# Optimization experiments

Measured on AMD Instinct MI355X. Metric: run time of the kernel, lower is better.

## Reference

```python
import jax, jax.numpy as jnp
import numpy as np

D = 1024
LD = 64
NTR = 8192
NT = 8192
DY = 128

def setup_inputs() -> dict:
    key = jax.random.key(0)
    k1, k2, k3, k4 = jax.random.split(key, 4)
    xtr = jax.random.normal(k1, (NTR, D), dtype=jnp.float32)
    ytr = jax.random.normal(k2, (NTR, DY), dtype=jnp.float32)
    xt = jax.random.normal(k3, (NT, D), dtype=jnp.float32)
    A = jax.random.normal(k4, (D, LD), dtype=jnp.float32) / (D ** 0.5)
    return {"xtr": xtr, "ytr": ytr, "xt": xt, "A": A}

def reference(xtr, ytr, xt, A):
    # mean-center both train and test features with the train mean
    mu = jnp.mean(xtr, axis=0, keepdims=True)          # [1, d]
    qtr = (xtr - mu) @ A                                # [Ntr, ld]
    qt = (xt - mu) @ A                                  # [Nt, ld]
    scores = jnp.einsum('nl,ml->nm', qt, qtr)           # [Nt, Ntr]
    E = jax.nn.softmax(scores, axis=1)                  # row-wise softmax over train points
    return E @ ytr                                      # [Nt, dy]
```

## Files before the change

kernel.cpp:

```cpp
#include <hip/hip_runtime.h>
#include <hip/hip_bf16.h>

#define D    1024
#define LD   64
#define NTR  8192
#define NT   8192
#define DY   128

#define SHIFT 40.0f
#define NCHUNK 8
#define CHUNK (NTR / NCHUNK)

typedef __attribute__((ext_vector_type(8))) short bf16x8;
typedef __attribute__((ext_vector_type(4))) short short4_;
typedef __attribute__((ext_vector_type(4))) float f4;

static __device__ __forceinline__ short f2bf(float f) {
    __hip_bfloat16 h = __float2bfloat16(f);
    short s; __builtin_memcpy(&s, &h, 2); return s;
}
static __device__ __forceinline__ float bf2f(short s) {
    __hip_bfloat16 h; __builtin_memcpy(&h, &s, 2); return __bfloat162float(h);
}

static __device__ __forceinline__ void gload_lds16(const void* g, void* l) {
    __builtin_amdgcn_global_load_lds(
        (const __attribute__((address_space(1))) unsigned int*)g,
        (__attribute__((address_space(3))) unsigned int*)l,
        16, 0, 0);
}

__global__ __launch_bounds__(256) void prep_all(const float* __restrict__ A,
                                                const float* __restrict__ ytr,
                                                short* __restrict__ AThi,
                                                short* __restrict__ ATlo,
                                                short* __restrict__ vtile) {
    __shared__ float tile[64][65];
    int b = blockIdx.x;
    if (b < 64) {
        int k = b * 16 + (threadIdx.x >> 4);
        int c0 = (threadIdx.x & 15) * 4;
        f4 a = *(const f4*)&A[(long)k * LD + c0];
        #pragma unroll
        for (int j = 0; j < 4; ++j) {
            int c = c0 + j;
            short hi = f2bf(a[j]);
            AThi[(long)c * D + k] = hi;
            ATlo[(long)c * D + k] = f2bf(a[j] - bf2f(hi));
        }
    } else {
        int bz = b - 64;
        int t0 = (bz & 127) * 64;
        int d0 = (bz >> 7) * 64;
        int c = threadIdx.x & 63;
        int r4 = threadIdx.x >> 6;
        #pragma unroll
        for (int i = 0; i < 16; ++i) {
            int r = i * 4 + r4;
            tile[r][c] = ytr[(long)(t0 + r) * DY + d0 + c];
        }
        __syncthreads();
        #pragma unroll
        for (int i = 0; i < 16; ++i) {
            int r = i * 4 + r4;
            int t = t0 + c;
            int dy = d0 + r;
            long idx = (long)(t >> 5) * 4096 + (long)dy * 32
                     + ((((t >> 3) & 3) ^ (dy & 3)) << 3) + (t & 7);
            vtile[idx] = f2bf(tile[c][r]);
        }
    }
}

__global__ __launch_bounds__(256) void proj_mfma(const float* __restrict__ xt,
                                                 const float* __restrict__ xtr,
                                                 const short* __restrict__ AThi,
                                                 const short* __restrict__ ATlo,
                                                 short* __restrict__ qt_hi,
                                                 short* __restrict__ qt_lo,
                                                 short* __restrict__ ktr_hi,
                                                 short* __restrict__ ktr_lo) {
    __shared__ __align__(16) float xbuf[2][1024];

    int tid = threadIdx.x;
    int wave = tid >> 6;
    int lane = tid & 63;
    int quad = lane >> 4;
    int l16 = lane & 15;

    int b = blockIdx.x;
    bool is_test = b < (NT / 16);
    int row0 = (is_test ? b : b - NT / 16) * 16;
    const float* x = is_test ? xt : xtr;

    int lr = wave * 4 + (lane >> 4);
    int cg = (lane & 15) ^ (lr & 7);
    const float* xsrc = x + (long)(row0 + lr) * D + cg * 4;
    float* ldst = &xbuf[0][wave * 256];

    const short* bhrow = AThi + (long)(wave * 16 + l16) * D + quad * 8;
    const short* blrow = ATlo + (long)(wave * 16 + l16) * D + quad * 8;

    f4 acc = (f4){0.f, 0.f, 0.f, 0.f};

    int pr0 = ((quad * 2) ^ (l16 & 7)) * 4;
    int pr1 = (((quad * 2) | 1) ^ (l16 & 7)) * 4;

    gload_lds16(xsrc, ldst);
    __syncthreads();

    #pragma unroll 1
    for (int s = 0; s < 16; ++s) {
        int cur = s & 1;
        if (s < 15)
            gload_lds16(xsrc + (s + 1) * 64, &xbuf[cur ^ 1][wave * 256]);

        const float* xrow = &xbuf[cur][l16 * 64];
        bf16x8 ah[2], al[2];
        #pragma unroll
        for (int h = 0; h < 2; ++h) {
            f4 v0 = *(const f4*)(xrow + h * 32 + pr0);
            f4 v1 = *(const f4*)(xrow + h * 32 + pr1);
            #pragma unroll
            for (int e = 0; e < 4; ++e) {
                short hi0 = f2bf(v0[e]);
                short hi1 = f2bf(v1[e]);
                ah[h][e]     = hi0;
                ah[h][e + 4] = hi1;
                al[h][e]     = f2bf(v0[e] - bf2f(hi0));
                al[h][e + 4] = f2bf(v1[e] - bf2f(hi1));
            }
        }
        int k0 = s * 64;
        bf16x8 bh0 = *(const bf16x8*)(bhrow + k0);
        bf16x8 bh1 = *(const bf16x8*)(bhrow + k0 + 32);
        bf16x8 bl0 = *(const bf16x8*)(blrow + k0);
        bf16x8 bl1 = *(const bf16x8*)(blrow + k0 + 32);
        acc = __builtin_amdgcn_mfma_f32_16x16x32_bf16(ah[0], bh0, acc, 0, 0, 0);
        acc = __builtin_amdgcn_mfma_f32_16x16x32_bf16(al[0], bh0, acc, 0, 0, 0);
        acc = __builtin_amdgcn_mfma_f32_16x16x32_bf16(ah[0], bl0, acc, 0, 0, 0);
        acc = __builtin_amdgcn_mfma_f32_16x16x32_bf16(ah[1], bh1, acc, 0, 0, 0);
        acc = __builtin_amdgcn_mfma_f32_16x16x32_bf16(al[1], bh1, acc, 0, 0, 0);
        acc = __builtin_amdgcn_mfma_f32_16x16x32_bf16(ah[1], bl1, acc, 0, 0, 0);

        __syncthreads();
    }


    int col = wave * 16 + l16;
    #pragma unroll
    for (int r = 0; r < 4; ++r) {
        int grow = row0 + quad * 4 + r;
        float qv = acc[r];
        short hi = f2bf(qv);
        short lo = f2bf(qv - bf2f(hi));
        if (is_test) {
            qt_hi[(long)grow * LD + col] = hi;
            qt_lo[(long)grow * LD + col] = lo;
        } else {
            int tl = grow & 31;
            long idx = (long)(grow >> 5) * 2048 + tl * 64
                     + ((((col >> 3) ^ (tl & 7))) << 3) + (col & 7);
            ktr_hi[idx] = hi;
            ktr_lo[idx] = lo;
        }
    }
}

__global__ __launch_bounds__(256) void muA_kernel(const short* __restrict__ ktr_hi,
                                                  const short* __restrict__ ktr_lo,
                                                  float* __restrict__ muA) {
    __shared__ float red[4][64];
    int l = threadIdx.x & 63;
    int g = threadIdx.x >> 6;
    float s = 0.f;
    #pragma unroll 2
    for (int tt = 0; tt < 4; ++tt) {
        long tb = (long)(blockIdx.x * 4 + tt) * 2048;
        #pragma unroll
        for (int tl = g * 8; tl < g * 8 + 8; ++tl) {
            long idx = tb + tl * 64 + ((((l >> 3) ^ (tl & 7))) << 3) + (l & 7);
            s += bf2f(ktr_hi[idx]) + bf2f(ktr_lo[idx]);
        }
    }
    red[g][l] = s;
    __syncthreads();
    if (threadIdx.x < 64)
        atomicAdd(&muA[l], (red[0][l] + red[1][l] + red[2][l] + red[3][l]) *
                               (1.0f / (float)NTR));
}

__global__ __launch_bounds__(256) void c_kernel(const short* __restrict__ ktr_hi,
                                                const short* __restrict__ ktr_lo,
                                                const float* __restrict__ muA,
                                                float* __restrict__ cc) {
    int t = blockIdx.x * 256 + threadIdx.x;
    int tl = t & 31;
    long rb = (long)(t >> 5) * 2048 + tl * 64;
    float s = SHIFT;
    #pragma unroll
    for (int c = 0; c < 8; ++c) {
        int pos = (c ^ (tl & 7)) << 3;
        bf16x8 h8 = *(const bf16x8*)&ktr_hi[rb + pos];
        bf16x8 l8 = *(const bf16x8*)&ktr_lo[rb + pos];
        f4 m0 = *(const f4*)&muA[c * 8];
        f4 m1 = *(const f4*)&muA[c * 8 + 4];
        #pragma unroll
        for (int j = 0; j < 4; ++j) {
            s += (bf2f(h8[j]) + bf2f(l8[j])) * m0[j];
            s += (bf2f(h8[j + 4]) + bf2f(l8[j + 4])) * m1[j];
        }
    }
    cc[t] = s;
}

__global__ __launch_bounds__(256, 2) void flash_kernel(const short* __restrict__ qt_hi,
                                                       const short* __restrict__ qt_lo,
                                                       const short* __restrict__ ksw_hi,
                                                       const short* __restrict__ ksw_lo,
                                                       const short* __restrict__ vtile,
                                                       const float* __restrict__ cc,
                                                       float* __restrict__ Opart,
                                                       float* __restrict__ Lpart) {
    __shared__ __align__(16) short kbh[2][2048];
    __shared__ __align__(16) short kbl[2][2048];
    __shared__ __align__(16) short vbuf[2][4096];
    __shared__ __align__(16) short ptile[4][1280];

    int tid = threadIdx.x;
    int wave = tid >> 6;
    int lane = tid & 63;
    int quad = lane >> 4;
    int l16 = lane & 15;

    int kc = blockIdx.x & 7;
    int qi = blockIdx.x >> 3;
    int q0w = qi * 128 + wave * 32;
    int tile0 = kc * 32;
    int kc0 = kc * CHUNK;

    int soff = wave * 512 + lane * 8;
    int ldso = wave * 512;

    bf16x8 qh[2][2], ql[2][2];
    #pragma unroll
    for (int rt = 0; rt < 2; ++rt) {
        const short* qrh = qt_hi + (long)(q0w + rt * 16 + l16) * LD + quad * 8;
        const short* qrl = qt_lo + (long)(q0w + rt * 16 + l16) * LD + quad * 8;
        qh[rt][0] = *(const bf16x8*)qrh;
        qh[rt][1] = *(const bf16x8*)(qrh + 32);
        ql[rt][0] = *(const bf16x8*)qrl;
        ql[rt][1] = *(const bf16x8*)(qrl + 32);
    }

    bf16x8 onef;
    #pragma unroll
    for (int i = 0; i < 8; ++i) onef[i] = (short)0x3F80;

    f4 Ov[2][8];
    f4 Lv[2];
    #pragma unroll
    for (int rt = 0; rt < 2; ++rt) {
        Lv[rt] = (f4){0.f, 0.f, 0.f, 0.f};
        #pragma unroll
        for (int jt = 0; jt < 8; ++jt) Ov[rt][jt] = (f4){0.f, 0.f, 0.f, 0.f};
    }

    short* myp = &ptile[wave][0];
    const int p0 = ((quad ^ (l16 & 7)) << 3);
    const int pv = ((quad ^ (l16 & 3)) << 3);

    gload_lds16(ksw_hi + (long)tile0 * 2048 + soff, &kbh[0][ldso]);
    gload_lds16(ksw_lo + (long)tile0 * 2048 + soff, &kbl[0][ldso]);
    gload_lds16(vtile + (long)tile0 * 4096 + soff, &vbuf[0][ldso]);
    gload_lds16(vtile + (long)tile0 * 4096 + 2048 + soff, &vbuf[0][2048 + ldso]);
    __syncthreads();

    #pragma unroll 1
    for (int it = 0; it < 32; ++it) {
        int cur = it & 1;

        f4 cv[2];
        #pragma unroll
        for (int tt = 0; tt < 2; ++tt)
            cv[tt] = *(const f4*)&cc[kc0 + it * 32 + tt * 16 + quad * 4];

        if (it < 31) {
            int nb = cur ^ 1;
            long tb = (long)(tile0 + it + 1);
            gload_lds16(ksw_hi + tb * 2048 + soff, &kbh[nb][ldso]);
            gload_lds16(ksw_lo + tb * 2048 + soff, &kbl[nb][ldso]);
            gload_lds16(vtile + tb * 4096 + soff, &vbuf[nb][ldso]);
            gload_lds16(vtile + tb * 4096 + 2048 + soff, &vbuf[nb][2048 + ldso]);
        }

        bf16x8 kh[2][2], kl[2][2];
        #pragma unroll
        for (int tt = 0; tt < 2; ++tt) {
            int rb = (tt * 16 + l16) * 64;
            kh[tt][0] = *(const bf16x8*)&kbh[cur][rb + p0];
            kh[tt][1] = *(const bf16x8*)&kbh[cur][rb + (p0 ^ 32)];
            kl[tt][0] = *(const bf16x8*)&kbl[cur][rb + p0];
            kl[tt][1] = *(const bf16x8*)&kbl[cur][rb + (p0 ^ 32)];
        }

        f4 s[2][2];
        #pragma unroll
        for (int rt = 0; rt < 2; ++rt) {
            #pragma unroll
            for (int tt = 0; tt < 2; ++tt) {
                f4 a = (f4){0.f, 0.f, 0.f, 0.f};
                a = __builtin_amdgcn_mfma_f32_16x16x32_bf16(kh[tt][0], qh[rt][0], a, 0, 0, 0);
                a = __builtin_amdgcn_mfma_f32_16x16x32_bf16(kh[tt][0], ql[rt][0], a, 0, 0, 0);
                a = __builtin_amdgcn_mfma_f32_16x16x32_bf16(kh[tt][1], qh[rt][1], a, 0, 0, 0);
                a = __builtin_amdgcn_mfma_f32_16x16x32_bf16(kh[tt][1], ql[rt][1], a, 0, 0, 0);
                a = __builtin_amdgcn_mfma_f32_16x16x32_bf16(kl[tt][0], qh[rt][0], a, 0, 0, 0);
                a = __builtin_amdgcn_mfma_f32_16x16x32_bf16(kl[tt][1], qh[rt][1], a, 0, 0, 0);
                s[rt][tt] = a;
            }
        }

        #pragma unroll
        for (int rt = 0; rt < 2; ++rt) {
            #pragma unroll
            for (int tt = 0; tt < 2; ++tt) {
                short4_ p4;
                p4[0] = f2bf(__expf(s[rt][tt][0] - cv[tt][0]));
                p4[1] = f2bf(__expf(s[rt][tt][1] - cv[tt][1]));
                p4[2] = f2bf(__expf(s[rt][tt][2] - cv[tt][2]));
                p4[3] = f2bf(__expf(s[rt][tt][3] - cv[tt][3]));
                *(short4_*)&myp[(rt * 16 + l16) * 40 + tt * 16 + quad * 4] = p4;
            }
        }

        bf16x8 vf[8];
        #pragma unroll
        for (int jt = 0; jt < 8; ++jt)
            vf[jt] = *(const bf16x8*)&vbuf[cur][(jt * 16 + l16) * 32 + pv];
        #pragma unroll
        for (int rt = 0; rt < 2; ++rt) {
            bf16x8 pf = *(const bf16x8*)&myp[(rt * 16 + l16) * 40 + quad * 8];
            #pragma unroll
            for (int jt = 0; jt < 8; ++jt)
                Ov[rt][jt] = __builtin_amdgcn_mfma_f32_16x16x32_bf16(pf, vf[jt], Ov[rt][jt], 0, 0, 0);
            Lv[rt] = __builtin_amdgcn_mfma_f32_16x16x32_bf16(pf, onef, Lv[rt], 0, 0, 0);
        }

        __syncthreads();
    }

    long ob = (long)kc * NT;
    #pragma unroll
    for (int rt = 0; rt < 2; ++rt) {
        #pragma unroll
        for (int jt = 0; jt < 8; ++jt) {
            #pragma unroll
            for (int r = 0; r < 4; ++r)
                Opart[(ob + q0w + rt * 16 + quad * 4 + r) * DY + jt * 16 + l16] =
                    Ov[rt][jt][r];
        }
        if (l16 == 0) {
            #pragma unroll
            for (int r = 0; r < 4; ++r)
                Lpart[ob + q0w + rt * 16 + quad * 4 + r] = Lv[rt][r];
        }
    }
}

__global__ __launch_bounds__(256) void finalize_kernel(const float* __restrict__ Opart,
                                                       const float* __restrict__ Lpart,
                                                       float* __restrict__ out) {
    long i = ((long)blockIdx.x * 256 + threadIdx.x) * 8;
    long row = i >> 7;
    float L = 0.f;
    f4 a = (f4){0.f, 0.f, 0.f, 0.f};
    f4 b = (f4){0.f, 0.f, 0.f, 0.f};
    #pragma unroll
    for (int kc = 0; kc < NCHUNK; ++kc) {
        L += Lpart[(long)kc * NT + row];
        const float* p = &Opart[((long)kc * NT) * DY + i];
        a += *(const f4*)p;
        b += *(const f4*)(p + 4);
    }
    float linv = 1.0f / L;
    a *= linv; b *= linv;
    *(f4*)&out[i] = a;
    *(f4*)&out[i + 4] = b;
}

extern "C" void kernel_launch(void* const* d_in, const int* in_sizes, int n_in,
                              void* d_out, int out_size, void* d_ws, size_t ws_size,
                              hipStream_t stream) {
    const float* xtr = (const float*)d_in[0];
    const float* ytr = (const float*)d_in[1];
    const float* xt  = (const float*)d_in[2];
    const float* A   = (const float*)d_in[3];
    float* out = (float*)d_out;

    char* w = (char*)d_ws;
    float* muA   = (float*)w; w += 4096;
    float* cc    = (float*)w; w += (size_t)NTR * 4;
    float* Lpart = (float*)w; w += (size_t)NCHUNK * NT * 4;
    float* Opart = (float*)w; w += (size_t)NCHUNK * NT * DY * 4;
    short* AThi  = (short*)w; w += (size_t)LD * D * 2;
    short* ATlo  = (short*)w; w += (size_t)LD * D * 2;
    short* qt_hi  = (short*)w; w += (size_t)NT * LD * 2;
    short* qt_lo  = (short*)w; w += (size_t)NT * LD * 2;
    short* ksw_hi = (short*)w; w += (size_t)NTR * LD * 2;
    short* ksw_lo = (short*)w; w += (size_t)NTR * LD * 2;
    short* vtile  = (short*)w; w += (size_t)DY * NTR * 2;
    (void)ws_size; (void)in_sizes; (void)n_in; (void)out_size;

    hipMemsetAsync(muA, 0, 4096, stream);
    prep_all<<<320, 256, 0, stream>>>(A, ytr, AThi, ATlo, vtile);
    proj_mfma<<<1024, 256, 0, stream>>>(xt, xtr, AThi, ATlo,
                                        qt_hi, qt_lo, ksw_hi, ksw_lo);
    muA_kernel<<<64, 256, 0, stream>>>(ksw_hi, ksw_lo, muA);
    c_kernel<<<32, 256, 0, stream>>>(ksw_hi, ksw_lo, muA, cc);
    flash_kernel<<<512, 256, 0, stream>>>(qt_hi, qt_lo, ksw_hi, ksw_lo, vtile, cc,
                                          Opart, Lpart);
    finalize_kernel<<<(NT * DY) / (256 * 8), 256, 0, stream>>>(Opart, Lpart, out);
}
```

Baseline: 195.4 us.

## Fuse prep, projection and mean reduction into one kernel, split A on the fly

Merges the A-split/ytr-transpose prep kernel with the projection kernel, so each projection block now converts A columns to bf16 hi/lo in registers instead of reading a precomputed transposed copy. The per-column train mean of projected keys is taken straight from accumulators as per-block partial sums, and c_kernel reduces them. This removes the memset, the muA_kernel launch and the atomics. In exchange, A is re-read with strided scalar loads and re-split by every block, which adds ALU work and uncoalesced reads in the projection loop.

Result: faster. 177.0 us (-9.4%).

```diff
diff --git a/kernel.cpp b/kernel.cpp
--- a/kernel.cpp
+++ b/kernel.cpp
@@ -30,34 +30,32 @@
         16, 0, 0);
 }
 
-__global__ __launch_bounds__(256) void prep_all(const float* __restrict__ A,
-                                                const float* __restrict__ ytr,
-                                                short* __restrict__ AThi,
-                                                short* __restrict__ ATlo,
-                                                short* __restrict__ vtile) {
-    __shared__ float tile[64][65];
+__global__ __launch_bounds__(256) void proj_prep(const float* __restrict__ xt,
+                                                 const float* __restrict__ xtr,
+                                                 const float* __restrict__ A,
+                                                 const float* __restrict__ ytr,
+                                                 short* __restrict__ qt_hi,
+                                                 short* __restrict__ qt_lo,
+                                                 short* __restrict__ ktr_hi,
+                                                 short* __restrict__ ktr_lo,
+                                                 float* __restrict__ muAp,
+                                                 short* __restrict__ vtile) {
+    __shared__ __align__(16) float smem[4224];
+
+    int tid = threadIdx.x;
     int b = blockIdx.x;
-    if (b < 64) {
-        int k = b * 16 + (threadIdx.x >> 4);
-        int c0 = (threadIdx.x & 15) * 4;
-        f4 a = *(const f4*)&A[(long)k * LD + c0];
-        #pragma unroll
-        for (int j = 0; j < 4; ++j) {
-            int c = c0 + j;
-            short hi = f2bf(a[j]);
-            AThi[(long)c * D + k] = hi;
-            ATlo[(long)c * D + k] = f2bf(a[j] - bf2f(hi));
-        }
-    } else {
-        int bz = b - 64;
+
+    if (b >= 1024) {
+        float* tile = smem;
+        int bz = b - 1024;
         int t0 = (bz & 127) * 64;
         int d0 = (bz >> 7) * 64;
-        int c = threadIdx.x & 63;
-        int r4 = threadIdx.x >> 6;
+        int c = tid & 63;
+        int r4 = tid >> 6;
         #pragma unroll
         for (int i = 0; i < 16; ++i) {
             int r = i * 4 + r4;
-            tile[r][c] = ytr[(long)(t0 + r) * DY + d0 + c];
+            tile[r * 66 + c] = ytr[(long)(t0 + r) * DY + d0 + c];
         }
         __syncthreads();
         #pragma unroll
@@ -67,28 +65,18 @@
             int dy = d0 + r;
             long idx = (long)(t >> 5) * 4096 + (long)dy * 32
                      + ((((t >> 3) & 3) ^ (dy & 3)) << 3) + (t & 7);
-            vtile[idx] = f2bf(tile[c][r]);
-        }
-    }
-}
-
-__global__ __launch_bounds__(256) void proj_mfma(const float* __restrict__ xt,
-                                                 const float* __restrict__ xtr,
-                                                 const short* __restrict__ AThi,
-                                                 const short* __restrict__ ATlo,
-                                                 short* __restrict__ qt_hi,
-                                                 short* __restrict__ qt_lo,
-                                                 short* __restrict__ ktr_hi,
-                                                 short* __restrict__ ktr_lo) {
-    __shared__ __align__(16) float xbuf[2][1024];
-
-    int tid = threadIdx.x;
+            vtile[idx] = f2bf(tile[c * 66 + r]);
+        }
+        return;
+    }
+
+    float (*xbuf)[2][1024] = (float (*)[2][1024])smem;
+
     int wave = tid >> 6;
     int lane = tid & 63;
     int quad = lane >> 4;
     int l16 = lane & 15;
 
-    int b = blockIdx.x;
     bool is_test = b < (NT / 16);
     int row0 = (is_test ? b : b - NT / 16) * 16;
     const float* x = is_test ? xt : xtr;
@@ -96,58 +84,69 @@
     int lr = wave * 4 + (lane >> 4);
     int cg = (lane & 15) ^ (lr & 7);
     const float* xsrc = x + (long)(row0 + lr) * D + cg * 4;
-    float* ldst = &xbuf[0][wave * 256];
-
-    const short* bhrow = AThi + (long)(wave * 16 + l16) * D + quad * 8;
-    const short* blrow = ATlo + (long)(wave * 16 + l16) * D + quad * 8;
+
+    int col = wave * 16 + l16;
+    const float* Acol = A + col;
 
     f4 acc = (f4){0.f, 0.f, 0.f, 0.f};
 
     int pr0 = ((quad * 2) ^ (l16 & 7)) * 4;
     int pr1 = (((quad * 2) | 1) ^ (l16 & 7)) * 4;
 
-    gload_lds16(xsrc, ldst);
+    gload_lds16(xsrc, &xbuf[0][0][wave * 256]);
+    gload_lds16(xsrc + 64, &xbuf[0][1][wave * 256]);
     __syncthreads();
 
     #pragma unroll 1
-    for (int s = 0; s < 16; ++s) {
+    for (int s = 0; s < 8; ++s) {
         int cur = s & 1;
-        if (s < 15)
-            gload_lds16(xsrc + (s + 1) * 64, &xbuf[cur ^ 1][wave * 256]);
-
-        const float* xrow = &xbuf[cur][l16 * 64];
-        bf16x8 ah[2], al[2];
-        #pragma unroll
-        for (int h = 0; h < 2; ++h) {
-            f4 v0 = *(const f4*)(xrow + h * 32 + pr0);
-            f4 v1 = *(const f4*)(xrow + h * 32 + pr1);
-            #pragma unroll
-            for (int e = 0; e < 4; ++e) {
-                short hi0 = f2bf(v0[e]);
-                short hi1 = f2bf(v1[e]);
-                ah[h][e]     = hi0;
-                ah[h][e + 4] = hi1;
-                al[h][e]     = f2bf(v0[e] - bf2f(hi0));
-                al[h][e + 4] = f2bf(v1[e] - bf2f(hi1));
+        if (s < 7) {
+            const float* nsrc = xsrc + (s + 1) * 128;
+            gload_lds16(nsrc, &xbuf[cur ^ 1][0][wave * 256]);
+            gload_lds16(nsrc + 64, &xbuf[cur ^ 1][1][wave * 256]);
+        }
+
+        #pragma unroll
+        for (int s2 = 0; s2 < 2; ++s2) {
+            int k0 = s * 128 + s2 * 64;
+
+            bf16x8 bh0, bh1, bl0, bl1;
+            #pragma unroll
+            for (int j = 0; j < 8; ++j) {
+                float a0 = Acol[(long)(k0 + quad * 8 + j) * LD];
+                float a1 = Acol[(long)(k0 + 32 + quad * 8 + j) * LD];
+                short h0 = f2bf(a0);
+                short h1 = f2bf(a1);
+                bh0[j] = h0; bl0[j] = f2bf(a0 - bf2f(h0));
+                bh1[j] = h1; bl1[j] = f2bf(a1 - bf2f(h1));
             }
-        }
-        int k0 = s * 64;
-        bf16x8 bh0 = *(const bf16x8*)(bhrow + k0);
-        bf16x8 bh1 = *(const bf16x8*)(bhrow + k0 + 32);
-        bf16x8 bl0 = *(const bf16x8*)(blrow + k0);
-        bf16x8 bl1 = *(const bf16x8*)(blrow + k0 + 32);
-        acc = __builtin_amdgcn_mfma_f32_16x16x32_bf16(ah[0], bh0, acc, 0, 0, 0);
-        acc = __builtin_amdgcn_mfma_f32_16x16x32_bf16(al[0], bh0, acc, 0, 0, 0);
-        acc = __builtin_amdgcn_mfma_f32_16x16x32_bf16(ah[0], bl0, acc, 0, 0, 0);
-        acc = __builtin_amdgcn_mfma_f32_16x16x32_bf16(ah[1], bh1, acc, 0, 0, 0);
-        acc = __builtin_amdgcn_mfma_f32_16x16x32_bf16(al[1], bh1, acc, 0, 0, 0);
-        acc = __builtin_amdgcn_mfma_f32_16x16x32_bf16(ah[1], bl1, acc, 0, 0, 0);
-
+
+            const float* xrow = &xbuf[cur][s2][l16 * 64];
+            bf16x8 ah[2], al[2];
+            #pragma unroll
+            for (int h = 0; h < 2; ++h) {
+                f4 v0 = *(const f4*)(xrow + h * 32 + pr0);
+                f4 v1 = *(const f4*)(xrow + h * 32 + pr1);
+                #pragma unroll
+                for (int e = 0; e < 4; ++e) {
+                    short hi0 = f2bf(v0[e]);
+                    short hi1 = f2bf(v1[e]);
+                    ah[h][e]     = hi0;
+                    ah[h][e + 4] = hi1;
+                    al[h][e]     = f2bf(v0[e] - bf2f(hi0));
+                    al[h][e + 4] = f2bf(v1[e] - bf2f(hi1));
+                }
+            }
+            acc = __builtin_amdgcn_mfma_f32_16x16x32_bf16(ah[0], bh0, acc, 0, 0, 0);
+            acc = __builtin_amdgcn_mfma_f32_16x16x32_bf16(al[0], bh0, acc, 0, 0, 0);
+            acc = __builtin_amdgcn_mfma_f32_16x16x32_bf16(ah[0], bl0, acc, 0, 0, 0);
+            acc = __builtin_amdgcn_mfma_f32_16x16x32_bf16(ah[1], bh1, acc, 0, 0, 0);
+            acc = __builtin_amdgcn_mfma_f32_16x16x32_bf16(al[1], bh1, acc, 0, 0, 0);
+            acc = __builtin_amdgcn_mfma_f32_16x16x32_bf16(ah[1], bl1, acc, 0, 0, 0);
+        }
         __syncthreads();
     }
 
-
-    int col = wave * 16 + l16;
     #pragma unroll
     for (int r = 0; r < 4; ++r) {
         int grow = row0 + quad * 4 + r;
@@ -165,35 +164,33 @@
             ktr_lo[idx] = lo;
         }
     }
-}
-
-__global__ __launch_bounds__(256) void muA_kernel(const short* __restrict__ ktr_hi,
-                                                  const short* __restrict__ ktr_lo,
-                                                  float* __restrict__ muA) {
+
+    if (!is_test) {
+        float s = acc[0] + acc[1] + acc[2] + acc[3];
+        s += __shfl_xor(s, 16);
+        s += __shfl_xor(s, 32);
+        if (quad == 0) muAp[(long)(b - NT / 16) * 64 + col] = s;
+    }
+}
+
+__global__ __launch_bounds__(256) void c_kernel(const short* __restrict__ ktr_hi,
+                                                const short* __restrict__ ktr_lo,
+                                                const float* __restrict__ muAp,
+                                                float* __restrict__ cc) {
     __shared__ float red[4][64];
+    __shared__ __align__(16) float muAs[64];
     int l = threadIdx.x & 63;
     int g = threadIdx.x >> 6;
-    float s = 0.f;
-    #pragma unroll 2
-    for (int tt = 0; tt < 4; ++tt) {
-        long tb = (long)(blockIdx.x * 4 + tt) * 2048;
-        #pragma unroll
-        for (int tl = g * 8; tl < g * 8 + 8; ++tl) {
-            long idx = tb + tl * 64 + ((((l >> 3) ^ (tl & 7))) << 3) + (l & 7);
-            s += bf2f(ktr_hi[idx]) + bf2f(ktr_lo[idx]);
-        }
-    }
-    red[g][l] = s;
+    float ms = 0.f;
+    #pragma unroll 8
+    for (int p = g; p < 512; p += 4) ms += muAp[(long)p * 64 + l];
+    red[g][l] = ms;
     __syncthreads();
     if (threadIdx.x < 64)
-        atomicAdd(&muA[l], (red[0][l] + red[1][l] + red[2][l] + red[3][l]) *
-                               (1.0f / (float)NTR));
-}
-
-__global__ __launch_bounds__(256) void c_kernel(const short* __restrict__ ktr_hi,
-                                                const short* __restrict__ ktr_lo,
-                                                const float* __restrict__ muA,
-                                                float* __restrict__ cc) {
+        muAs[l] = (red[0][l] + red[1][l] + red[2][l] + red[3][l]) *
+                  (1.0f / (float)NTR);
+    __syncthreads();
+
     int t = blockIdx.x * 256 + threadIdx.x;
     int tl = t & 31;
     long rb = (long)(t >> 5) * 2048 + tl * 64;
@@ -203,8 +200,8 @@
         int pos = (c ^ (tl & 7)) << 3;
         bf16x8 h8 = *(const bf16x8*)&ktr_hi[rb + pos];
         bf16x8 l8 = *(const bf16x8*)&ktr_lo[rb + pos];
-        f4 m0 = *(const f4*)&muA[c * 8];
-        f4 m1 = *(const f4*)&muA[c * 8 + 4];
+        f4 m0 = *(const f4*)&muAs[c * 8];
+        f4 m1 = *(const f4*)&muAs[c * 8 + 4];
         #pragma unroll
         for (int j = 0; j < 4; ++j) {
             s += (bf2f(h8[j]) + bf2f(l8[j])) * m0[j];
@@ -398,12 +395,10 @@
     float* out = (float*)d_out;
 
     char* w = (char*)d_ws;
-    float* muA   = (float*)w; w += 4096;
+    float* muAp  = (float*)w; w += (size_t)512 * 64 * 4;
     float* cc    = (float*)w; w += (size_t)NTR * 4;
     float* Lpart = (float*)w; w += (size_t)NCHUNK * NT * 4;
     float* Opart = (float*)w; w += (size_t)NCHUNK * NT * DY * 4;
-    short* AThi  = (short*)w; w += (size_t)LD * D * 2;
-    short* ATlo  = (short*)w; w += (size_t)LD * D * 2;
     short* qt_hi  = (short*)w; w += (size_t)NT * LD * 2;
     short* qt_lo  = (short*)w; w += (size_t)NT * LD * 2;
     short* ksw_hi = (short*)w; w += (size_t)NTR * LD * 2;
@@ -411,12 +406,9 @@
     short* vtile  = (short*)w; w += (size_t)DY * NTR * 2;
     (void)ws_size; (void)in_sizes; (void)n_in; (void)out_size;
 
-    hipMemsetAsync(muA, 0, 4096, stream);
-    prep_all<<<320, 256, 0, stream>>>(A, ytr, AThi, ATlo, vtile);
-    proj_mfma<<<1024, 256, 0, stream>>>(xt, xtr, AThi, ATlo,
-                                        qt_hi, qt_lo, ksw_hi, ksw_lo);
-    muA_kernel<<<64, 256, 0, stream>>>(ksw_hi, ksw_lo, muA);
-    c_kernel<<<32, 256, 0, stream>>>(ksw_hi, ksw_lo, muA, cc);
+    proj_prep<<<1280, 256, 0, stream>>>(xt, xtr, A, ytr,
+                                        qt_hi, qt_lo, ksw_hi, ksw_lo, muAp, vtile);
+    c_kernel<<<32, 256, 0, stream>>>(ksw_hi, ksw_lo, muAp, cc);
     flash_kernel<<<512, 256, 0, stream>>>(qt_hi, qt_lo, ksw_hi, ksw_lo, vtile, cc,
                                           Opart, Lpart);
     finalize_kernel<<<(NT * DY) / (256 * 8), 256, 0, stream>>>(Opart, Lpart, out);
```
